# Kernel optimization log

Hardware: AMD Instinct MI355X
Metric: run time of the kernel (lower is better)

The kernel has to match this reference:

```python
import jax, jax.numpy as jnp
import numpy as np

NUM_HEADS = 8


def _ln(x, w, b, eps=1e-5):
    mu = x.mean(-1, keepdims=True)
    var = ((x - mu) ** 2).mean(-1, keepdims=True)
    return (x - mu) * jax.lax.rsqrt(var + eps) * w + b


def _qkv(x, w, H, d):
    # x: (n, l, C) -> q,k,v each (n, H, l, d)
    n, l, _ = x.shape
    qkv = (x @ w.T).reshape(n, l, 3, H, d)
    qkv = jnp.transpose(qkv, (2, 0, 3, 1, 4))
    return qkv[0], qkv[1], qkv[2]


def _qkv_head(x, w, d):
    # x: (n, H, l, d) -> q,k,v each (n, H, l, d); linear acts on head_dim
    n, H, l, _ = x.shape
    qkv = (x @ w.T).reshape(n, H, l, 3, d)
    qkv = jnp.transpose(qkv, (3, 0, 1, 2, 4))
    return qkv[0], qkv[1], qkv[2]


def _attn(q, k, v, scale):
    s = jax.nn.softmax(jnp.einsum('nhqd,nhkd->nhqk', q, k) * scale, axis=-1)
    return jnp.einsum('nhqk,nhkd->nhqd', s, v)


def setup_inputs() -> dict:
    key = jax.random.key(0)
    ks = jax.random.split(key, 10)
    B, N, C = 16, 4096, 512
    l = 64
    H, d = NUM_HEADS, C // NUM_HEADS
    return {
        'x': jax.random.normal(ks[0], (B, N, C), jnp.float32),
        'n3_w': jnp.ones((C,), jnp.float32),
        'n3_b': jnp.zeros((C,), jnp.float32),
        'n4_w': jnp.ones((C,), jnp.float32),
        'n4_b': jnp.zeros((C,), jnp.float32),
        'ln1_w': jax.random.normal(ks[1], (3 * C, C), jnp.float32) * 0.02,
        'ln2_w': jax.random.normal(ks[2], (3 * C, C), jnp.float32) * 0.02,
        'ln3_w': jax.random.normal(ks[3], (3 * d, d), jnp.float32) * 0.02,
        'ln4_w': jax.random.normal(ks[4], (3 * d, d), jnp.float32) * 0.02,
        'pos1': jax.random.normal(ks[5], (1, l, C), jnp.float32),
        'pos2': jax.random.normal(ks[6], (1, l, C), jnp.float32),
        'pos3': jax.random.normal(ks[7], (1, H, l, d), jnp.float32),
        'pos4': jax.random.normal(ks[8], (1, H, l, d), jnp.float32),
    }


def reference(x, n3_w, n3_b, n4_w, n4_b, ln1_w, ln2_w, ln3_w, ln4_w,
              pos1, pos2, pos3, pos4):
    B, N, C = x.shape
    l = int(np.sqrt(N))
    H = NUM_HEADS
    d = C // H
    scale = d ** -0.5

    # window (row) branch
    x_w = _ln(x, n3_w, n3_b).reshape(B * l, l, C) + pos1
    q, k, v = _qkv(x_w, ln1_w, H, d)
    x_ww = _attn(q, k, v, scale) + pos3                     # (B*l, H, l, d)
    xw_q, xw_k, xw_v = _qkv_head(x_ww, ln3_w, d)

    # height (column) branch: transpose the l x l grid
    x_h = _ln(x, n4_w, n4_b).reshape(B, l, l, C)
    x_h = jnp.swapaxes(x_h, 1, 2).reshape(B * l, l, C) + pos2
    q, k, v = _qkv(x_h, ln2_w, H, d)
    x_hh = _attn(q, k, v, scale) + pos4
    xh_q, xh_k, xh_v = _qkv_head(x_hh, ln4_w, d)

    # cross-attention between the two axial branches
    o1 = _attn(xh_q, xw_k, xw_v, scale)                     # (B*l, H, l, d)
    o1 = jnp.swapaxes(o1, 1, 2).reshape(B, l, l, C)
    o1 = jnp.swapaxes(o1, 1, 2)
    o2 = _attn(xw_q, xh_k, xh_v, scale)
    o2 = jnp.swapaxes(o2, 1, 2).reshape(B, l, l, C)

    out = (o1 + o2).reshape(B, N, C) + x
    return out
```

## Files before the change

kernel.cpp:

```cpp
#include <hip/hip_runtime.h>

typedef unsigned short u16;
typedef __attribute__((ext_vector_type(8))) short bf16x8;
typedef __attribute__((ext_vector_type(4))) float floatx4;
typedef __attribute__((ext_vector_type(4))) unsigned short u16x4;

__device__ __forceinline__ float b2f(u16 u) {
  unsigned int i = ((unsigned int)u) << 16;
  return __builtin_bit_cast(float, i);
}
__device__ __forceinline__ u16 f2b(float f) {
  unsigned int i = __builtin_bit_cast(unsigned int, f);
  i += 0x7fffu + ((i >> 16) & 1u);
  return (u16)(i >> 16);
}
#define MFMA16(a, b, c) __builtin_amdgcn_mfma_f32_16x16x32_bf16((a), (b), (c), 0, 0, 0)
#define LGKM0() __asm__ volatile("s_waitcnt lgkmcnt(0)" ::: "memory")
#define VM0() __asm__ volatile("s_waitcnt vmcnt(0)" ::: "memory")

__device__ __forceinline__ void gload_lds16(const u16* g, u16* l) {
  __builtin_amdgcn_global_load_lds(
      (const __attribute__((address_space(1))) void*)g,
      (__attribute__((address_space(3))) void*)l, 16, 0, 0);
}

__global__ __launch_bounds__(256) void cvt_kernel(const float* __restrict__ a,
                                                  u16* __restrict__ o, int n4) {
  int i = blockIdx.x * 256 + threadIdx.x;
  if (i < n4) {
    float4 v = ((const float4*)a)[i];
    u16x4 r;
    r.x = f2b(v.x); r.y = f2b(v.y); r.z = f2b(v.z); r.w = f2b(v.w);
    ((u16x4*)o)[i] = r;
  }
}

__global__ __launch_bounds__(256) void ln_pos_kernel(
    const float* __restrict__ x, const float* __restrict__ n3w, const float* __restrict__ n3b,
    const float* __restrict__ n4w, const float* __restrict__ n4b,
    const float* __restrict__ pos1, const float* __restrict__ pos2,
    u16* __restrict__ yW, u16* __restrict__ yH) {
  int wv = threadIdx.x >> 6, lane = threadIdx.x & 63;
  int token = blockIdx.x * 4 + wv;
  int b = token >> 12, r = (token >> 6) & 63, c = token & 63;
  const float4* xr = (const float4*)(x + (size_t)token * 512) + lane * 2;
  float4 x0 = xr[0], x1 = xr[1];
  float v[8] = {x0.x, x0.y, x0.z, x0.w, x1.x, x1.y, x1.z, x1.w};
  float s = 0.f, ss = 0.f;
#pragma unroll
  for (int j = 0; j < 8; j++) { s += v[j]; ss += v[j] * v[j]; }
#pragma unroll
  for (int off = 1; off < 64; off <<= 1) { s += __shfl_xor(s, off); ss += __shfl_xor(ss, off); }
  float mu = s * (1.0f / 512.0f);
  float var = ss * (1.0f / 512.0f) - mu * mu;
  float rs = rsqrtf(var + 1e-5f);
  int ch0 = lane * 8;
  float w3[8], b3[8], w4[8], b4[8], p1[8], p2[8];
  *(float4*)&w3[0] = *(const float4*)(n3w + ch0); *(float4*)&w3[4] = *(const float4*)(n3w + ch0 + 4);
  *(float4*)&b3[0] = *(const float4*)(n3b + ch0); *(float4*)&b3[4] = *(const float4*)(n3b + ch0 + 4);
  *(float4*)&w4[0] = *(const float4*)(n4w + ch0); *(float4*)&w4[4] = *(const float4*)(n4w + ch0 + 4);
  *(float4*)&b4[0] = *(const float4*)(n4b + ch0); *(float4*)&b4[4] = *(const float4*)(n4b + ch0 + 4);
  const float* p1p = pos1 + (size_t)c * 512 + ch0;
  const float* p2p = pos2 + (size_t)r * 512 + ch0;
  *(float4*)&p1[0] = *(const float4*)p1p; *(float4*)&p1[4] = *(const float4*)(p1p + 4);
  *(float4*)&p2[0] = *(const float4*)p2p; *(float4*)&p2[4] = *(const float4*)(p2p + 4);
  bf16x8 ow, oh;
#pragma unroll
  for (int j = 0; j < 8; j++) {
    float xn = (v[j] - mu) * rs;
    ow[j] = (short)f2b(xn * w3[j] + b3[j] + p1[j]);
    oh[j] = (short)f2b(xn * w4[j] + b4[j] + p2[j]);
  }
  *(bf16x8*)(yW + (size_t)token * 512 + ch0) = ow;
  size_t hrow = (size_t)b * 4096 + (size_t)c * 64 + r;
  *(bf16x8*)(yH + hrow * 512 + ch0) = oh;
}

__global__ __launch_bounds__(256) void qkv_gemm_kernel(
    const u16* __restrict__ A0, const u16* __restrict__ A1,
    const u16* __restrict__ W0, const u16* __restrict__ W1,
    u16* __restrict__ Z0, u16* __restrict__ Z1) {
  const int K = 512, N = 1536;
  int br = blockIdx.z;
  const u16* A = br ? A1 : A0;
  const u16* W = br ? W1 : W0;
  u16* Z = br ? Z1 : Z0;
  int lin = blockIdx.y * 12 + blockIdx.x;
  int nl = (lin & 7) * 768 + (lin >> 3);
  int n0 = (nl % 12) * 128, m0 = (nl / 12) * 128;
  __shared__ u16 gpool[16384];
  int tid = threadIdx.x, lane = tid & 63, wave = tid >> 6;
  int wm = (wave >> 1) * 64, wn = (wave & 1) * 64;
  int ml = lane & 15, quad = lane >> 4;
  floatx4 acc[4][4];
#pragma unroll
  for (int mi = 0; mi < 4; mi++)
#pragma unroll
    for (int ni = 0; ni < 4; ni++) acc[mi][ni] = (floatx4){0.f, 0.f, 0.f, 0.f};

  int srow = (lane >> 2);
  int scol = (lane & 3) * 8;
  {
    u16 (*As)[32] = (u16(*)[32])gpool;
    u16 (*Bs)[32] = (u16(*)[32])(gpool + 4096);
#pragma unroll
    for (int i = 0; i < 2; i++) {
      int rbase = wave * 32 + i * 16;
      gload_lds16(A + (size_t)(m0 + rbase + srow) * K + scol, &As[rbase][0]);
      gload_lds16(W + (size_t)(n0 + rbase + srow) * K + scol, &Bs[rbase][0]);
    }
  }
  VM0();
  __syncthreads();
  for (int t = 0; t < 16; ++t) {
    u16* cb = gpool + (t & 1) * 8192;
    u16* nb = gpool + ((t & 1) ^ 1) * 8192;
    if (t < 15) {
      int kt = (t + 1) * 32;
      u16 (*As)[32] = (u16(*)[32])nb;
      u16 (*Bs)[32] = (u16(*)[32])(nb + 4096);
#pragma unroll
      for (int i = 0; i < 2; i++) {
        int rbase = wave * 32 + i * 16;
        gload_lds16(A + (size_t)(m0 + rbase + srow) * K + kt + scol, &As[rbase][0]);
        gload_lds16(W + (size_t)(n0 + rbase + srow) * K + kt + scol, &Bs[rbase][0]);
      }
    }
    u16 (*Asc)[32] = (u16(*)[32])cb;
    u16 (*Bsc)[32] = (u16(*)[32])(cb + 4096);
    bf16x8 a[4], bfr[4];
#pragma unroll
    for (int mi = 0; mi < 4; mi++) a[mi] = *(const bf16x8*)&Asc[wm + mi * 16 + ml][quad * 8];
#pragma unroll
    for (int ni = 0; ni < 4; ni++) bfr[ni] = *(const bf16x8*)&Bsc[wn + ni * 16 + ml][quad * 8];
#pragma unroll
    for (int mi = 0; mi < 4; mi++)
#pragma unroll
      for (int ni = 0; ni < 4; ni++) acc[mi][ni] = MFMA16(a[mi], bfr[ni], acc[mi][ni]);
    VM0();
    __syncthreads();
  }
  u16* wl = gpool + wave * 2048;
#pragma unroll
  for (int pair = 0; pair < 2; pair++) {
#pragma unroll
    for (int mh = 0; mh < 2; mh++) {
      int mi = pair * 2 + mh;
#pragma unroll
      for (int ni = 0; ni < 4; ni++)
#pragma unroll
        for (int r = 0; r < 4; r++)
          wl[(mh * 16 + quad * 4 + r) * 64 + ni * 16 + ml] = f2b(acc[mi][ni][r]);
    }
    LGKM0();
#pragma unroll
    for (int p = 0; p < 4; p++) {
      int lrow = p * 8 + (lane >> 3);
      int col8 = (lane & 7) * 8;
      bf16x8 vv = *(const bf16x8*)&wl[lrow * 64 + col8];
      int rg = m0 + wm + pair * 32 + lrow;
      *(bf16x8*)&Z[(size_t)rg * N + n0 + wn + col8] = vv;
    }
    LGKM0();
  }
}

__device__ __forceinline__ void attn_core(bf16x8 aq0, bf16x8 aq1,
                                          const u16 (*Ks)[72], const u16 (*Vt)[72],
                                          u16 (*Psw)[72], int lane, floatx4 o[4]) {
  int ml = lane & 15, quad = lane >> 4;
  floatx4 s[4];
#pragma unroll
  for (int nt = 0; nt < 4; nt++) {
    floatx4 z = (floatx4){0.f, 0.f, 0.f, 0.f};
    bf16x8 b0 = *(const bf16x8*)&Ks[nt * 16 + ml][quad * 8];
    bf16x8 b1 = *(const bf16x8*)&Ks[nt * 16 + ml][32 + quad * 8];
    z = MFMA16(aq0, b0, z);
    z = MFMA16(aq1, b1, z);
    s[nt] = z;
  }
#pragma unroll
  for (int r = 0; r < 4; r++) {
    float m = -1e30f;
#pragma unroll
    for (int nt = 0; nt < 4; nt++) { s[nt][r] *= 0.125f; m = fmaxf(m, s[nt][r]); }
#pragma unroll
    for (int off = 1; off < 16; off <<= 1) m = fmaxf(m, __shfl_xor(m, off));
    float su = 0.f;
#pragma unroll
    for (int nt = 0; nt < 4; nt++) { float p = __expf(s[nt][r] - m); s[nt][r] = p; su += p; }
#pragma unroll
    for (int off = 1; off < 16; off <<= 1) su += __shfl_xor(su, off);
    float inv = 1.0f / su;
#pragma unroll
    for (int nt = 0; nt < 4; nt++) s[nt][r] *= inv;
  }
#pragma unroll
  for (int nt = 0; nt < 4; nt++)
#pragma unroll
    for (int r = 0; r < 4; r++) Psw[quad * 4 + r][nt * 16 + ml] = f2b(s[nt][r]);
  LGKM0();
  bf16x8 ap0 = *(const bf16x8*)&Psw[ml][quad * 8];
  bf16x8 ap1 = *(const bf16x8*)&Psw[ml][32 + quad * 8];
#pragma unroll
  for (int et = 0; et < 4; et++) {
    floatx4 z = (floatx4){0.f, 0.f, 0.f, 0.f};
    bf16x8 b0 = *(const bf16x8*)&Vt[et * 16 + ml][quad * 8];
    bf16x8 b1 = *(const bf16x8*)&Vt[et * 16 + ml][32 + quad * 8];
    z = MFMA16(ap0, b0, z);
    z = MFMA16(ap1, b1, z);
    o[et] = z;
  }
}

__device__ __forceinline__ void head_qkv(const floatx4 o[4], const float* pp,
                                         const u16* lw, u16 (*Ks)[72], u16 (*Vt)[72],
                                         u16 (*Ps)[72], int wv, int lane,
                                         bf16x8& axq0, bf16x8& axq1) {
  int ml = lane & 15, quad = lane >> 4;
#pragma unroll
  for (int et = 0; et < 4; et++)
#pragma unroll
    for (int r = 0; r < 4; r++) {
      int qp = wv * 16 + quad * 4 + r, e = et * 16 + ml;
      Ps[quad * 4 + r][et * 16 + ml] = f2b(o[et][r] + pp[(size_t)qp * 64 + e]);
    }
  LGKM0();
  bf16x8 ax0 = *(const bf16x8*)&Ps[ml][quad * 8];
  bf16x8 ax1 = *(const bf16x8*)&Ps[ml][32 + quad * 8];
  LGKM0();
  __builtin_amdgcn_sched_barrier(0);
#pragma unroll
  for (int nj = 0; nj < 4; nj++) {
    int col = 64 + nj * 16 + ml;
    bf16x8 b0 = *(const bf16x8*)(lw + (size_t)col * 64 + quad * 8);
    bf16x8 b1 = *(const bf16x8*)(lw + (size_t)col * 64 + 32 + quad * 8);
    floatx4 z = (floatx4){0.f, 0.f, 0.f, 0.f};
    z = MFMA16(ax0, b0, z);
    z = MFMA16(ax1, b1, z);
#pragma unroll
    for (int r = 0; r < 4; r++)
      Ks[wv * 16 + quad * 4 + r][nj * 16 + ml] = f2b(z[r]);
  }
#pragma unroll
  for (int nj = 0; nj < 4; nj++) {
    int col = 128 + nj * 16 + ml;
    bf16x8 b0 = *(const bf16x8*)(lw + (size_t)col * 64 + quad * 8);
    bf16x8 b1 = *(const bf16x8*)(lw + (size_t)col * 64 + 32 + quad * 8);
    floatx4 z = (floatx4){0.f, 0.f, 0.f, 0.f};
    z = MFMA16(ax0, b0, z);
    z = MFMA16(ax1, b1, z);
#pragma unroll
    for (int r = 0; r < 4; r++)
      Vt[nj * 16 + ml][wv * 16 + quad * 4 + r] = f2b(z[r]);
  }
#pragma unroll
  for (int nj = 0; nj < 4; nj++) {
    int col = nj * 16 + ml;
    bf16x8 b0 = *(const bf16x8*)(lw + (size_t)col * 64 + quad * 8);
    bf16x8 b1 = *(const bf16x8*)(lw + (size_t)col * 64 + 32 + quad * 8);
    floatx4 z = (floatx4){0.f, 0.f, 0.f, 0.f};
    z = MFMA16(ax0, b0, z);
    z = MFMA16(ax1, b1, z);
#pragma unroll
    for (int r = 0; r < 4; r++)
      Ps[quad * 4 + r][nj * 16 + ml] = f2b(z[r]);
  }
  LGKM0();
  __builtin_amdgcn_sched_barrier(0);
  axq0 = *(const bf16x8*)&Ps[ml][quad * 8];
  axq1 = *(const bf16x8*)&Ps[ml][32 + quad * 8];
  LGKM0();
}

__global__ __launch_bounds__(256) void fused_attn_kernel(
    const u16* __restrict__ Zw, const u16* __restrict__ Zh,
    const u16* __restrict__ l3b, const u16* __restrict__ l4b,
    const float* __restrict__ pos3, const float* __restrict__ pos4,
    u16* __restrict__ o1b, u16* __restrict__ o2b) {
  int w = blockIdx.x, h = blockIdx.y;
  __shared__ u16 pool[23040];
  u16 (*KsW)[72] = (u16(*)[72])pool;
  u16 (*VtW)[72] = (u16(*)[72])(pool + 4608);
  u16 (*KsH)[72] = (u16(*)[72])(pool + 9216);
  u16 (*VtH)[72] = (u16(*)[72])(pool + 13824);
  int tid = threadIdx.x, lane = tid & 63, wv = tid >> 6;
  int ml = lane & 15, quad = lane >> 4;
  u16 (*Ps)[72] = (u16(*)[72])(pool + 18432 + wv * 1152);
  const u16* baseW = Zw + (size_t)w * 64 * 1536 + h * 64;
  const u16* baseH = Zh + (size_t)w * 64 * 1536 + h * 64;
  for (int i = tid; i < 512; i += 256) {
    int r = i >> 3, c = (i & 7) * 8;
    *(bf16x8*)&KsW[r][c] = *(const bf16x8*)(baseW + 512 + (size_t)r * 1536 + c);
    *(bf16x8*)&KsH[r][c] = *(const bf16x8*)(baseH + 512 + (size_t)r * 1536 + c);
  }
  for (int i = tid; i < 1024; i += 256) {
    int p = i >> 4, e0 = (i & 15) * 4;
    u16x4 vW = *(const u16x4*)(baseW + 1024 + (size_t)p * 1536 + e0);
    u16x4 vH = *(const u16x4*)(baseH + 1024 + (size_t)p * 1536 + e0);
    VtW[e0 + 0][p] = vW.x; VtW[e0 + 1][p] = vW.y; VtW[e0 + 2][p] = vW.z; VtW[e0 + 3][p] = vW.w;
    VtH[e0 + 0][p] = vH.x; VtH[e0 + 1][p] = vH.y; VtH[e0 + 2][p] = vH.z; VtH[e0 + 3][p] = vH.w;
  }
  const u16* qrW = baseW + (size_t)(wv * 16 + ml) * 1536 + quad * 8;
  const u16* qrH = baseH + (size_t)(wv * 16 + ml) * 1536 + quad * 8;
  bf16x8 aqW0 = *(const bf16x8*)qrW;
  bf16x8 aqW1 = *(const bf16x8*)(qrW + 32);
  bf16x8 aqH0 = *(const bf16x8*)qrH;
  bf16x8 aqH1 = *(const bf16x8*)(qrH + 32);
  __syncthreads();
  floatx4 oW[4], oH[4];
  attn_core(aqW0, aqW1, KsW, VtW, Ps, lane, oW);
  attn_core(aqH0, aqH1, KsH, VtH, Ps, lane, oH);
  __syncthreads();
  bf16x8 axqW0, axqW1, axqH0, axqH1;
  head_qkv(oW, pos3 + (size_t)h * 4096, l3b, KsW, VtW, Ps, wv, lane, axqW0, axqW1);
  __syncthreads();
  head_qkv(oH, pos4 + (size_t)h * 4096, l4b, KsH, VtH, Ps, wv, lane, axqH0, axqH1);
  __syncthreads();
  floatx4 c2[4], c1[4];
  attn_core(axqW0, axqW1, KsH, VtH, Ps, lane, c2);
  attn_core(axqH0, axqH1, KsW, VtW, Ps, lane, c1);
  __syncthreads();
  u16* Out1 = pool;
  u16* Out2 = pool + 4608;
#pragma unroll
  for (int et = 0; et < 4; et++)
#pragma unroll
    for (int r = 0; r < 4; r++) {
      int row = wv * 16 + quad * 4 + r;
      Out1[row * 64 + et * 16 + ml] = f2b(c1[et][r]);
      Out2[row * 64 + et * 16 + ml] = f2b(c2[et][r]);
    }
  __syncthreads();
  u16* o1p = o1b + (size_t)w * 32768 + h * 64;
  u16* o2p = o2b + (size_t)w * 32768 + h * 64;
#pragma unroll
  for (int j = 0; j < 2; j++) {
    int c = tid + j * 256;
    int pos = c >> 3, cc = (c & 7) * 8;
    *(bf16x8*)&o1p[(size_t)pos * 512 + cc] = *(const bf16x8*)&Out1[pos * 64 + cc];
    *(bf16x8*)&o2p[(size_t)pos * 512 + cc] = *(const bf16x8*)&Out2[pos * 64 + cc];
  }
}

__global__ __launch_bounds__(256) void final_add_kernel(
    const float* __restrict__ x, const u16* __restrict__ o1b,
    const u16* __restrict__ o2b, float* __restrict__ out) {
  int wv = threadIdx.x >> 6, lane = threadIdx.x & 63;
  int token = blockIdx.x * 4 + wv;
  int b = token >> 12, r = (token >> 6) & 63, c = token & 63;
  size_t i = (size_t)token * 512 + lane * 8;
  size_t i1 = ((size_t)b * 4096 + (size_t)c * 64 + r) * 512 + lane * 8;
  float vx[8];
  *(float4*)&vx[0] = *(const float4*)(x + i);
  *(float4*)&vx[4] = *(const float4*)(x + i + 4);
  bf16x8 v1 = *(const bf16x8*)(o1b + i1);
  bf16x8 v2 = *(const bf16x8*)(o2b + i);
  float vo[8];
#pragma unroll
  for (int j = 0; j < 8; j++)
    vo[j] = vx[j] + b2f((u16)v1[j]) + b2f((u16)v2[j]);
  *(float4*)(out + i) = *(float4*)&vo[0];
  *(float4*)(out + i + 4) = *(float4*)&vo[4];
}

extern "C" void kernel_launch(void* const* d_in, const int* in_sizes, int n_in,
                              void* d_out, int out_size, void* d_ws, size_t ws_size,
                              hipStream_t stream) {
  const float* x    = (const float*)d_in[0];
  const float* n3w  = (const float*)d_in[1];
  const float* n3b  = (const float*)d_in[2];
  const float* n4w  = (const float*)d_in[3];
  const float* n4b  = (const float*)d_in[4];
  const float* ln1  = (const float*)d_in[5];
  const float* ln2  = (const float*)d_in[6];
  const float* ln3  = (const float*)d_in[7];
  const float* ln4  = (const float*)d_in[8];
  const float* pos1 = (const float*)d_in[9];
  const float* pos2 = (const float*)d_in[10];
  const float* pos3 = (const float*)d_in[11];
  const float* pos4 = (const float*)d_in[12];

  char* ws = (char*)d_ws;
  u16* yW = (u16*)ws;
  u16* yH = (u16*)(ws + (size_t)67108864);
  u16* Zw = (u16*)(ws + (size_t)134217728);
  u16* Zh = (u16*)(ws + (size_t)335544320);
  u16* o1b = yW;
  u16* o2b = yH;
  float* out = (float*)d_out;

  u16* Wb1 = (u16*)d_out;
  u16* Wb2 = Wb1 + 786432;
  u16* l3b = Wb2 + 786432;
  u16* l4b = l3b + 12288;

  cvt_kernel<<<768, 256, 0, stream>>>(ln1, Wb1, 196608);
  cvt_kernel<<<768, 256, 0, stream>>>(ln2, Wb2, 196608);
  cvt_kernel<<<12, 256, 0, stream>>>(ln3, l3b, 3072);
  cvt_kernel<<<12, 256, 0, stream>>>(ln4, l4b, 3072);
  ln_pos_kernel<<<16384, 256, 0, stream>>>(x, n3w, n3b, n4w, n4b, pos1, pos2, yW, yH);
  qkv_gemm_kernel<<<dim3(12, 512, 2), 256, 0, stream>>>(yW, yH, Wb1, Wb2, Zw, Zh);
  fused_attn_kernel<<<dim3(1024, 8), 256, 0, stream>>>(Zw, Zh, l3b, l4b, pos3, pos4, o1b, o2b);
  final_add_kernel<<<16384, 256, 0, stream>>>(x, o1b, o2b, out);
}
```

Baseline: 898.2 us.

## Split window and height branches across two wave groups in fused attention

The fused attention block grows from 256 to 512 threads. The first four waves handle the window branch and the last four handle the height branch, so the two branch attention and head-QKV steps run in parallel instead of one after the other. Each half loads only its own K/V and writes one output. This adds more waves per block and extra LDS for the per-wave P scratch, which could lower the number of resident blocks per CU.

```diff
diff --git a/kernel.cpp b/kernel.cpp
--- a/kernel.cpp
+++ b/kernel.cpp
@@ -215,14 +215,14 @@
 
 __device__ __forceinline__ void head_qkv(const floatx4 o[4], const float* pp,
                                          const u16* lw, u16 (*Ks)[72], u16 (*Vt)[72],
-                                         u16 (*Ps)[72], int wv, int lane,
+                                         u16 (*Ps)[72], int wr, int lane,
                                          bf16x8& axq0, bf16x8& axq1) {
   int ml = lane & 15, quad = lane >> 4;
 #pragma unroll
   for (int et = 0; et < 4; et++)
 #pragma unroll
     for (int r = 0; r < 4; r++) {
-      int qp = wv * 16 + quad * 4 + r, e = et * 16 + ml;
+      int qp = wr * 16 + quad * 4 + r, e = et * 16 + ml;
       Ps[quad * 4 + r][et * 16 + ml] = f2b(o[et][r] + pp[(size_t)qp * 64 + e]);
     }
   LGKM0();
@@ -240,7 +240,7 @@
     z = MFMA16(ax1, b1, z);
 #pragma unroll
     for (int r = 0; r < 4; r++)
-      Ks[wv * 16 + quad * 4 + r][nj * 16 + ml] = f2b(z[r]);
+      Ks[wr * 16 + quad * 4 + r][nj * 16 + ml] = f2b(z[r]);
   }
 #pragma unroll
   for (int nj = 0; nj < 4; nj++) {
@@ -252,7 +252,7 @@
     z = MFMA16(ax1, b1, z);
 #pragma unroll
     for (int r = 0; r < 4; r++)
-      Vt[nj * 16 + ml][wv * 16 + quad * 4 + r] = f2b(z[r]);
+      Vt[nj * 16 + ml][wr * 16 + quad * 4 + r] = f2b(z[r]);
   }
 #pragma unroll
   for (int nj = 0; nj < 4; nj++) {
@@ -273,73 +273,74 @@
   LGKM0();
 }
 
-__global__ __launch_bounds__(256) void fused_attn_kernel(
+__global__ __launch_bounds__(512) void fused_attn_kernel(
     const u16* __restrict__ Zw, const u16* __restrict__ Zh,
     const u16* __restrict__ l3b, const u16* __restrict__ l4b,
     const float* __restrict__ pos3, const float* __restrict__ pos4,
     u16* __restrict__ o1b, u16* __restrict__ o2b) {
   int w = blockIdx.x, h = blockIdx.y;
-  __shared__ u16 pool[23040];
+  __shared__ u16 pool[27648];
   u16 (*KsW)[72] = (u16(*)[72])pool;
   u16 (*VtW)[72] = (u16(*)[72])(pool + 4608);
   u16 (*KsH)[72] = (u16(*)[72])(pool + 9216);
   u16 (*VtH)[72] = (u16(*)[72])(pool + 13824);
   int tid = threadIdx.x, lane = tid & 63, wv = tid >> 6;
+  int bw = wv >> 2;
+  int wr = wv & 3;
+  int gt = tid & 255;
   int ml = lane & 15, quad = lane >> 4;
   u16 (*Ps)[72] = (u16(*)[72])(pool + 18432 + wv * 1152);
   const u16* baseW = Zw + (size_t)w * 64 * 1536 + h * 64;
   const u16* baseH = Zh + (size_t)w * 64 * 1536 + h * 64;
-  for (int i = tid; i < 512; i += 256) {
+  const u16* base = bw ? baseH : baseW;
+  u16 (*Ks)[72] = bw ? KsH : KsW;
+  u16 (*Vt)[72] = bw ? VtH : VtW;
+  u16 (*Ko)[72] = bw ? KsW : KsH;
+  u16 (*Vo)[72] = bw ? VtW : VtH;
+  for (int i = gt; i < 512; i += 256) {
     int r = i >> 3, c = (i & 7) * 8;
-    *(bf16x8*)&KsW[r][c] = *(const bf16x8*)(baseW + 512 + (size_t)r * 1536 + c);
-    *(bf16x8*)&KsH[r][c] = *(const bf16x8*)(baseH + 512 + (size_t)r * 1536 + c);
-  }
-  for (int i = tid; i < 1024; i += 256) {
+    *(bf16x8*)&Ks[r][c] = *(const bf16x8*)(base + 512 + (size_t)r * 1536 + c);
+  }
+  for (int i = gt; i < 1024; i += 256) {
     int p = i >> 4, e0 = (i & 15) * 4;
-    u16x4 vW = *(const u16x4*)(baseW + 1024 + (size_t)p * 1536 + e0);
-    u16x4 vH = *(const u16x4*)(baseH + 1024 + (size_t)p * 1536 + e0);
-    VtW[e0 + 0][p] = vW.x; VtW[e0 + 1][p] = vW.y; VtW[e0 + 2][p] = vW.z; VtW[e0 + 3][p] = vW.w;
-    VtH[e0 + 0][p] = vH.x; VtH[e0 + 1][p] = vH.y; VtH[e0 + 2][p] = vH.z; VtH[e0 + 3][p] = vH.w;
-  }
-  const u16* qrW = baseW + (size_t)(wv * 16 + ml) * 1536 + quad * 8;
-  const u16* qrH = baseH + (size_t)(wv * 16 + ml) * 1536 + quad * 8;
-  bf16x8 aqW0 = *(const bf16x8*)qrW;
-  bf16x8 aqW1 = *(const bf16x8*)(qrW + 32);
-  bf16x8 aqH0 = *(const bf16x8*)qrH;
-  bf16x8 aqH1 = *(const bf16x8*)(qrH + 32);
-  __syncthreads();
-  floatx4 oW[4], oH[4];
-  attn_core(aqW0, aqW1, KsW, VtW, Ps, lane, oW);
-  attn_core(aqH0, aqH1, KsH, VtH, Ps, lane, oH);
-  __syncthreads();
-  bf16x8 axqW0, axqW1, axqH0, axqH1;
-  head_qkv(oW, pos3 + (size_t)h * 4096, l3b, KsW, VtW, Ps, wv, lane, axqW0, axqW1);
-  __syncthreads();
-  head_qkv(oH, pos4 + (size_t)h * 4096, l4b, KsH, VtH, Ps, wv, lane, axqH0, axqH1);
-  __syncthreads();
-  floatx4 c2[4], c1[4];
-  attn_core(axqW0, axqW1, KsH, VtH, Ps, lane, c2);
-  attn_core(axqH0, axqH1, KsW, VtW, Ps, lane, c1);
+    u16x4 vv = *(const u16x4*)(base + 1024 + (size_t)p * 1536 + e0);
+    Vt[e0 + 0][p] = vv.x; Vt[e0 + 1][p] = vv.y; Vt[e0 + 2][p] = vv.z; Vt[e0 + 3][p] = vv.w;
+  }
+  const u16* qr = base + (size_t)(wr * 16 + ml) * 1536 + quad * 8;
+  bf16x8 aq0 = *(const bf16x8*)qr;
+  bf16x8 aq1 = *(const bf16x8*)(qr + 32);
+  __syncthreads();
+  floatx4 o[4];
+  attn_core(aq0, aq1, Ks, Vt, Ps, lane, o);
+  __syncthreads();
+  const float* pp = (bw ? pos4 : pos3) + (size_t)h * 4096;
+  const u16* lw = bw ? l4b : l3b;
+  bf16x8 axq0, axq1;
+  head_qkv(o, pp, lw, Ks, Vt, Ps, wr, lane, axq0, axq1);
+  __syncthreads();
+  floatx4 c[4];
+  attn_core(axq0, axq1, Ko, Vo, Ps, lane, c);
   __syncthreads();
   u16* Out1 = pool;
   u16* Out2 = pool + 4608;
+  u16* OutMine = bw ? Out1 : Out2;
 #pragma unroll
   for (int et = 0; et < 4; et++)
 #pragma unroll
     for (int r = 0; r < 4; r++) {
-      int row = wv * 16 + quad * 4 + r;
-      Out1[row * 64 + et * 16 + ml] = f2b(c1[et][r]);
-      Out2[row * 64 + et * 16 + ml] = f2b(c2[et][r]);
+      int row = wr * 16 + quad * 4 + r;
+      OutMine[row * 64 + et * 16 + ml] = f2b(c[et][r]);
     }
   __syncthreads();
   u16* o1p = o1b + (size_t)w * 32768 + h * 64;
   u16* o2p = o2b + (size_t)w * 32768 + h * 64;
+  u16* dst = bw ? o1p : o2p;
+  const u16* src = bw ? Out1 : Out2;
 #pragma unroll
   for (int j = 0; j < 2; j++) {
-    int c = tid + j * 256;
-    int pos = c >> 3, cc = (c & 7) * 8;
-    *(bf16x8*)&o1p[(size_t)pos * 512 + cc] = *(const bf16x8*)&Out1[pos * 64 + cc];
-    *(bf16x8*)&o2p[(size_t)pos * 512 + cc] = *(const bf16x8*)&Out2[pos * 64 + cc];
+    int cidx = gt + j * 256;
+    int pos = cidx >> 3, cc = (cidx & 7) * 8;
+    *(bf16x8*)&dst[(size_t)pos * 512 + cc] = *(const bf16x8*)&src[pos * 64 + cc];
   }
 }
 
@@ -401,6 +402,6 @@
   cvt_kernel<<<12, 256, 0, stream>>>(ln4, l4b, 3072);
   ln_pos_kernel<<<16384, 256, 0, stream>>>(x, n3w, n3b, n4w, n4b, pos1, pos2, yW, yH);
   qkv_gemm_kernel<<<dim3(12, 512, 2), 256, 0, stream>>>(yW, yH, Wb1, Wb2, Zw, Zh);
-  fused_attn_kernel<<<dim3(1024, 8), 256, 0, stream>>>(Zw, Zh, l3b, l4b, pos3, pos4, o1b, o2b);
+  fused_attn_kernel<<<dim3(1024, 8), 512, 0, stream>>>(Zw, Zh, l3b, l4b, pos3, pos4, o1b, o2b);
   final_add_kernel<<<16384, 256, 0, stream>>>(x, o1b, o2b, out);
 }
```

New measurement: 939.8 us. 1.05x slower.
